# Performance work log

Hardware: AMD Instinct MI355X
Metric: run time of the kernel (lower is better)

Reference implementation:

```python
import jax, jax.numpy as jnp
import numpy as np

NB_FEAT = 20000
NB_CLASSES = 30
N_EDGES = 640000
BATCH = 128


def setup_inputs() -> dict:
    key = jax.random.key(0)
    k1, k2, k3, k4, k5 = jax.random.split(key, 5)
    x = jax.random.normal(k1, (BATCH, NB_FEAT), dtype=jnp.float32)
    edge_index = jax.random.randint(k2, (2, N_EDGES), 0, NB_FEAT, dtype=jnp.int64)
    edge_weight = jax.random.uniform(k3, (N_EDGES,), dtype=jnp.float32)
    fc_w = jax.random.normal(k4, (NB_CLASSES, NB_FEAT), dtype=jnp.float32) * 0.01
    fc_b = jax.random.normal(k5, (NB_CLASSES,), dtype=jnp.float32) * 0.01
    return {"x": x, "edge_index": edge_index, "edge_weight": edge_weight,
            "fc_w": fc_w, "fc_b": fc_b}


def reference(x, edge_index, edge_weight, fc_w, fc_b):
    # SGConv(K=1, bias=False, lin.weight frozen to 1) == gcn_norm + one propagation.
    B, N = x.shape
    src, dst = edge_index[0], edge_index[1]
    # add self-loops with weight 1 (gcn_norm default fill_value=1)
    loop = jnp.arange(N)
    src_f = jnp.concatenate([src, loop])
    dst_f = jnp.concatenate([dst, loop])
    w_f = jnp.concatenate([edge_weight, jnp.ones((N,), edge_weight.dtype)])
    # symmetric normalization: deg over target index
    deg = jax.ops.segment_sum(w_f, dst_f, num_segments=N)  # (N,)
    dinv = jnp.where(deg > 0, jax.lax.rsqrt(deg), 0.0)
    wn = dinv[src_f] * w_f * dinv[dst_f]  # (E',)
    # batched gather-multiply-scatter; graph shared across batch, so vectorize over B
    msgs = x[:, src_f] * wn  # (B, E')
    diffused = jax.ops.segment_sum(msgs.T, dst_f, num_segments=N).T  # (B, N)
    # dropout p=0 -> no-op; dense FC + softmax
    logits = diffused @ fc_w.T + fc_b  # (B, C)
    return jax.nn.softmax(logits, axis=1)
```

## Files before the change

kernel.cpp:

```cpp
#include <hip/hip_runtime.h>


#define N_NODES   20000
#define N_EDGES_C 640000
#define N_CLASSES 30
#define CPAD      32

#define HBLKS     32
#define HNODES    10000
#define HEDGES    (N_EDGES_C / HBLKS)

#define BN        32
#define NB        625
#define NSLAB     256
#define SLAB_E    (N_EDGES_C / NSLAB)
#define ECAP      1440

#define XLD       129
#define GTLD      33

__global__ __launch_bounds__(512) void k1_histscatter(const int* __restrict__ src,
        const int* __restrict__ dst, const float* __restrict__ ew,
        float* __restrict__ degp, int* __restrict__ gcur,
        int2* __restrict__ erec) {
    __shared__ union {
        float h[HNODES];
        struct { int ssrc[SLAB_E]; int shist[NB]; int scur[NB]; } s;
    } sm;
    int bid = blockIdx.x;
    int t = threadIdx.x;
    if (bid < 2 * HBLKS) {
        int eb = bid >> 1, half = bid & 1;
        int nbase = half * HNODES;
        for (int i = t; i < HNODES; i += 512) sm.h[i] = 0.f;
        __syncthreads();
        const int4* d4 = (const int4*)(dst + eb * HEDGES);
        const float4* w4 = (const float4*)(ew + eb * HEDGES);
        for (int i = t; i < HEDGES / 4; i += 512) {
            int4 dv = d4[i]; float4 wv = w4[i];
            unsigned r;
            r = (unsigned)(dv.x - nbase); if (r < HNODES) atomicAdd(&sm.h[r], wv.x);
            r = (unsigned)(dv.y - nbase); if (r < HNODES) atomicAdd(&sm.h[r], wv.y);
            r = (unsigned)(dv.z - nbase); if (r < HNODES) atomicAdd(&sm.h[r], wv.z);
            r = (unsigned)(dv.w - nbase); if (r < HNODES) atomicAdd(&sm.h[r], wv.w);
        }
        __syncthreads();
        float* outp = degp + (size_t)bid * HNODES;
        for (int i = t; i < HNODES; i += 512) outp[i] = sm.h[i];
    } else {
        int slab = bid - 2 * HBLKS;
        int e0 = slab * SLAB_E;
        for (int i = t; i < NB; i += 512) sm.s.shist[i] = 0;
        __syncthreads();
        const int4* s4 = (const int4*)(src + e0);
        for (int i = t; i < SLAB_E / 4; i += 512) {
            int4 sv = s4[i];
            ((int4*)sm.s.ssrc)[i] = sv;
            atomicAdd(&sm.s.shist[sv.x >> 5], 1);
            atomicAdd(&sm.s.shist[sv.y >> 5], 1);
            atomicAdd(&sm.s.shist[sv.z >> 5], 1);
            atomicAdd(&sm.s.shist[sv.w >> 5], 1);
        }
        __syncthreads();
        for (int b = t; b < NB; b += 512)
            sm.s.scur[b] = b * ECAP + atomicAdd(&gcur[b], sm.s.shist[b]);
        __syncthreads();
        const int4* d4 = (const int4*)(dst + e0);
        const float4* w4 = (const float4*)(ew + e0);
        for (int i = t; i < SLAB_E / 4; i += 512) {
            int4 dv = d4[i]; float4 wv = w4[i];
            int4 sv = ((const int4*)sm.s.ssrc)[i];
            int s, p;
            s = sv.x; p = atomicAdd(&sm.s.scur[s >> 5], 1);
            erec[p] = make_int2(((s & 31) << 15) | dv.x, __float_as_int(wv.x));
            s = sv.y; p = atomicAdd(&sm.s.scur[s >> 5], 1);
            erec[p] = make_int2(((s & 31) << 15) | dv.y, __float_as_int(wv.y));
            s = sv.z; p = atomicAdd(&sm.s.scur[s >> 5], 1);
            erec[p] = make_int2(((s & 31) << 15) | dv.z, __float_as_int(wv.z));
            s = sv.w; p = atomicAdd(&sm.s.scur[s >> 5], 1);
            erec[p] = make_int2(((s & 31) << 15) | dv.w, __float_as_int(wv.w));
        }
    }
}

__global__ __launch_bounds__(256) void k2_prep(const float* __restrict__ degp,
        const float* __restrict__ fc_w, float* __restrict__ dinv,
        float* __restrict__ fcT) {
    __shared__ float tile[CPAD][BN + 1];
    __shared__ float sdinv[BN];
    int n0 = blockIdx.x * BN;
    int t = threadIdx.x;
    if (t < BN) {
        int n = n0 + t;
        int half = n / HNODES, nn = n - half * HNODES;
        float s = 1.0f;
        for (int eb = 0; eb < HBLKS; eb++)
            s += degp[(size_t)((eb << 1) | half) * HNODES + nn];
        float di = rsqrtf(s);
        dinv[n] = di;
        sdinv[t] = di;
    }
    #pragma unroll
    for (int k = 0; k < 4; k++) {
        int idx = k * 256 + t;
        int c = idx >> 5, nn = idx & 31;
        tile[c][nn] = (c < N_CLASSES) ? fc_w[c * N_NODES + n0 + nn] : 0.f;
    }
    __syncthreads();
    #pragma unroll
    for (int k = 0; k < 4; k++) {
        int idx = k * 256 + t;
        int nn = idx >> 5, c = idx & 31;
        fcT[(size_t)(n0 + nn) * CPAD + c] = sdinv[nn] * tile[c][nn];
    }
}

__global__ __launch_bounds__(512) void k3_foldgemm(const int2* __restrict__ erec,
        const int* __restrict__ gcur, const float* __restrict__ dinv,
        const float* __restrict__ fcT, const float* __restrict__ x,
        float* __restrict__ part) {
    __shared__ union {
        struct { int2 srt[ECAP]; int hist[BN]; int rowst[BN]; int cur[BN]; } f;
        struct { float xl[BN * XLD]; float gt[CPAD * GTLD]; } g;
    } sm;
    float* gt = sm.g.gt;
    int bucket = blockIdx.x;
    int t = threadIdx.x;
    int nlo = bucket * BN;
    int bstart = bucket * ECAP;
    int len = min(gcur[bucket], ECAP);

    if (t < BN) sm.f.hist[t] = 0;
    __syncthreads();
    for (int i = t; i < len; i += 512)
        atomicAdd(&sm.f.hist[((unsigned)erec[bstart + i].x) >> 15], 1);
    __syncthreads();
    if (t < BN) {
        int h = sm.f.hist[t];
        int v = h;
        #pragma unroll
        for (int o = 1; o < BN; o <<= 1) {
            int u = __shfl_up(v, o, BN);
            if (t >= o) v += u;
        }
        sm.f.rowst[t] = v - h;
        sm.f.cur[t]   = v - h;
    }
    __syncthreads();
    for (int i = t; i < len; i += 512) {
        int2 r = erec[bstart + i];
        int p = atomicAdd(&sm.f.cur[((unsigned)r.x) >> 15], 1);
        sm.f.srt[p] = r;
    }
    __syncthreads();

    int c = t & 31;
    int grp = t >> 5;
    #pragma unroll
    for (int half = 0; half < 2; half++) {
        int nn = grp + half * 16;
        int n = nlo + nn;
        float acc  = fcT[(size_t)n * CPAD + c];
        float acc2 = 0.f;
        int i = sm.f.rowst[nn], re = i + sm.f.hist[nn];
        for (; i + 1 < re; i += 2) {
            int2 r0 = sm.f.srt[i], r1 = sm.f.srt[i + 1];
            acc  += __int_as_float(r0.y) * fcT[(size_t)(r0.x & 0x7FFF) * CPAD + c];
            acc2 += __int_as_float(r1.y) * fcT[(size_t)(r1.x & 0x7FFF) * CPAD + c];
        }
        if (i < re) {
            int2 r0 = sm.f.srt[i];
            acc += __int_as_float(r0.y) * fcT[(size_t)(r0.x & 0x7FFF) * CPAD + c];
        }
        gt[c * GTLD + nn] = dinv[n] * (acc + acc2);
    }
    __syncthreads();

    for (int o = t; o < 128 * BN; o += 512) {
        int b = o >> 5, n = o & 31;
        sm.g.xl[n * XLD + b] = x[(size_t)b * N_NODES + nlo + n];
    }
    __syncthreads();

    int wv = t >> 6, l = t & 63;
    float a00 = 0.f, a01 = 0.f, a10 = 0.f, a11 = 0.f;
    float a20 = 0.f, a21 = 0.f, a30 = 0.f, a31 = 0.f;
    #pragma unroll 8
    for (int n = 0; n < BN; n++) {
        float x0 = sm.g.xl[n * XLD + l];
        float x1 = sm.g.xl[n * XLD + 64 + l];
        float g0 = gt[(wv)      * GTLD + n];
        float g1 = gt[(wv +  8) * GTLD + n];
        float g2 = gt[(wv + 16) * GTLD + n];
        float g3 = gt[(wv + 24) * GTLD + n];
        a00 += x0 * g0; a01 += x1 * g0;
        a10 += x0 * g1; a11 += x1 * g1;
        a20 += x0 * g2; a21 += x1 * g2;
        a30 += x0 * g3; a31 += x1 * g3;
    }
    float* pb = part + (size_t)bucket * CPAD * 128;
    pb[(wv)      * 128 + l]      = a00;
    pb[(wv)      * 128 + 64 + l] = a01;
    pb[(wv +  8) * 128 + l]      = a10;
    pb[(wv +  8) * 128 + 64 + l] = a11;
    pb[(wv + 16) * 128 + l]      = a20;
    pb[(wv + 16) * 128 + 64 + l] = a21;
    pb[(wv + 24) * 128 + l]      = a30;
    pb[(wv + 24) * 128 + 64 + l] = a31;
}

__global__ __launch_bounds__(128) void k4_lred(const float* __restrict__ part,
        float* __restrict__ lpart) {
    int c = blockIdx.x, q = blockIdx.y;
    int b = threadIdx.x;
    float s = 0.f;
    for (int ch = q; ch < NB; ch += 5)
        s += part[(size_t)ch * CPAD * 128 + c * 128 + b];
    lpart[(q * CPAD + c) * 128 + b] = s;
}

__global__ void k5_smax(const float* __restrict__ lpart,
        const float* __restrict__ fc_b, float* __restrict__ out) {
    int b = threadIdx.x;
    float v[N_CLASSES], m = -1e30f;
    #pragma unroll
    for (int c = 0; c < N_CLASSES; c++) {
        float s = fc_b[c];
        #pragma unroll
        for (int q = 0; q < 5; q++) s += lpart[(q * CPAD + c) * 128 + b];
        v[c] = s; m = fmaxf(m, s);
    }
    float s = 0.f;
    #pragma unroll
    for (int c = 0; c < N_CLASSES; c++) { v[c] = __expf(v[c] - m); s += v[c]; }
    float inv = 1.0f / s;
    #pragma unroll
    for (int c = 0; c < N_CLASSES; c++) out[b * N_CLASSES + c] = v[c] * inv;
}

extern "C" void kernel_launch(void* const* d_in, const int* in_sizes, int n_in,
                              void* d_out, int out_size, void* d_ws, size_t ws_size,
                              hipStream_t stream) {
    const float* x          = (const float*)d_in[0];
    const int*   edge_index = (const int*)d_in[1];
    const float* ew         = (const float*)d_in[2];
    const float* fc_w       = (const float*)d_in[3];
    const float* fc_b       = (const float*)d_in[4];
    float* out = (float*)d_out;

    const int* src = edge_index;
    const int* dst = edge_index + N_EDGES_C;

    float* A     = (float*)d_ws;
    int2*  erec  = (int2*)(A + (size_t)NB * CPAD * 128);
    float* dinv  = (float*)(erec + (size_t)NB * ECAP);
    int*   gcur  = (int*)(dinv + N_NODES);
    float* fcT   = (float*)(gcur + 640);
    float* lpart = fcT + (size_t)N_NODES * CPAD;

    float* degp = A;
    float* part = A;

    hipMemsetAsync(gcur, 0, 640 * sizeof(int), stream);

    k1_histscatter<<<2 * HBLKS + NSLAB, 512, 0, stream>>>(src, dst, ew, degp,
                                                          gcur, erec);
    k2_prep<<<NB, 256, 0, stream>>>(degp, fc_w, dinv, fcT);
    k3_foldgemm<<<NB, 512, 0, stream>>>(erec, gcur, dinv, fcT, x, part);
    k4_lred<<<dim3(N_CLASSES, 5), 128, 0, stream>>>(part, lpart);
    k5_smax<<<1, 128, 0, stream>>>(lpart, fc_b, out);
}
```

Measured before the change: 96.14 us.

## Retune slab count, unroll gather by four, relayout partials, replace memset kernel

Raises the edge-slab block count in the histogram/scatter kernel, widens the k3 gather loop to four independent accumulators, and changes the partial-sum layout to class-major so each class's chunks are contiguous. The class reduction now runs over all chunks in one block per class and adds the bias there, leaving softmax to read finished logits. The memset is replaced by a tiny init kernel. Together these target launch overhead, latency hiding in the gather, and reduction access patterns. The trade-off is that the reduction uses only 30 blocks, giving less parallelism.

```diff
diff --git a/kernel.cpp b/kernel.cpp
--- a/kernel.cpp
+++ b/kernel.cpp
@@ -12,12 +12,17 @@
 
 #define BN        32
 #define NB        625
-#define NSLAB     256
+#define NSLAB     500
 #define SLAB_E    (N_EDGES_C / NSLAB)
 #define ECAP      1440
 
 #define XLD       129
 #define GTLD      33
+
+__global__ void k0_init(int* __restrict__ gcur) {
+    int t = threadIdx.x;
+    if (t < NB) gcur[t] = 0;
+}
 
 __global__ __launch_bounds__(512) void k1_histscatter(const int* __restrict__ src,
         const int* __restrict__ dst, const float* __restrict__ ew,
@@ -160,19 +165,22 @@
     for (int half = 0; half < 2; half++) {
         int nn = grp + half * 16;
         int n = nlo + nn;
-        float acc  = fcT[(size_t)n * CPAD + c];
-        float acc2 = 0.f;
+        float a0 = fcT[(size_t)n * CPAD + c];
+        float a1 = 0.f, a2 = 0.f, a3 = 0.f;
         int i = sm.f.rowst[nn], re = i + sm.f.hist[nn];
-        for (; i + 1 < re; i += 2) {
+        for (; i + 3 < re; i += 4) {
             int2 r0 = sm.f.srt[i], r1 = sm.f.srt[i + 1];
-            acc  += __int_as_float(r0.y) * fcT[(size_t)(r0.x & 0x7FFF) * CPAD + c];
-            acc2 += __int_as_float(r1.y) * fcT[(size_t)(r1.x & 0x7FFF) * CPAD + c];
-        }
-        if (i < re) {
+            int2 r2 = sm.f.srt[i + 2], r3 = sm.f.srt[i + 3];
+            a0 += __int_as_float(r0.y) * fcT[(size_t)(r0.x & 0x7FFF) * CPAD + c];
+            a1 += __int_as_float(r1.y) * fcT[(size_t)(r1.x & 0x7FFF) * CPAD + c];
+            a2 += __int_as_float(r2.y) * fcT[(size_t)(r2.x & 0x7FFF) * CPAD + c];
+            a3 += __int_as_float(r3.y) * fcT[(size_t)(r3.x & 0x7FFF) * CPAD + c];
+        }
+        for (; i < re; i++) {
             int2 r0 = sm.f.srt[i];
-            acc += __int_as_float(r0.y) * fcT[(size_t)(r0.x & 0x7FFF) * CPAD + c];
-        }
-        gt[c * GTLD + nn] = dinv[n] * (acc + acc2);
+            a0 += __int_as_float(r0.y) * fcT[(size_t)(r0.x & 0x7FFF) * CPAD + c];
+        }
+        gt[c * GTLD + nn] = dinv[n] * ((a0 + a1) + (a2 + a3));
     }
     __syncthreads();
 
@@ -198,37 +206,36 @@
         a20 += x0 * g2; a21 += x1 * g2;
         a30 += x0 * g3; a31 += x1 * g3;
     }
-    float* pb = part + (size_t)bucket * CPAD * 128;
-    pb[(wv)      * 128 + l]      = a00;
-    pb[(wv)      * 128 + 64 + l] = a01;
-    pb[(wv +  8) * 128 + l]      = a10;
-    pb[(wv +  8) * 128 + 64 + l] = a11;
-    pb[(wv + 16) * 128 + l]      = a20;
-    pb[(wv + 16) * 128 + 64 + l] = a21;
-    pb[(wv + 24) * 128 + l]      = a30;
-    pb[(wv + 24) * 128 + 64 + l] = a31;
+    part[((size_t)(wv)      * NB + bucket) * 128 + l]      = a00;
+    part[((size_t)(wv)      * NB + bucket) * 128 + 64 + l] = a01;
+    part[((size_t)(wv +  8) * NB + bucket) * 128 + l]      = a10;
+    part[((size_t)(wv +  8) * NB + bucket) * 128 + 64 + l] = a11;
+    part[((size_t)(wv + 16) * NB + bucket) * 128 + l]      = a20;
+    part[((size_t)(wv + 16) * NB + bucket) * 128 + 64 + l] = a21;
+    part[((size_t)(wv + 24) * NB + bucket) * 128 + l]      = a30;
+    part[((size_t)(wv + 24) * NB + bucket) * 128 + 64 + l] = a31;
 }
 
 __global__ __launch_bounds__(128) void k4_lred(const float* __restrict__ part,
-        float* __restrict__ lpart) {
-    int c = blockIdx.x, q = blockIdx.y;
+        const float* __restrict__ fc_b, float* __restrict__ logits_g) {
+    int c = blockIdx.x;
     int b = threadIdx.x;
+    const float* p = part + (size_t)c * NB * 128 + b;
     float s = 0.f;
-    for (int ch = q; ch < NB; ch += 5)
-        s += part[(size_t)ch * CPAD * 128 + c * 128 + b];
-    lpart[(q * CPAD + c) * 128 + b] = s;
-}
-
-__global__ void k5_smax(const float* __restrict__ lpart,
-        const float* __restrict__ fc_b, float* __restrict__ out) {
+    #pragma unroll 8
+    for (int ch = 0; ch < NB; ch++)
+        s += p[(size_t)ch * 128];
+    logits_g[b * CPAD + c] = s + fc_b[c];
+}
+
+__global__ void k5_smax(const float* __restrict__ logits_g,
+        float* __restrict__ out) {
     int b = threadIdx.x;
     float v[N_CLASSES], m = -1e30f;
     #pragma unroll
     for (int c = 0; c < N_CLASSES; c++) {
-        float s = fc_b[c];
-        #pragma unroll
-        for (int q = 0; q < 5; q++) s += lpart[(q * CPAD + c) * 128 + b];
-        v[c] = s; m = fmaxf(m, s);
+        v[c] = logits_g[b * CPAD + c];
+        m = fmaxf(m, v[c]);
     }
     float s = 0.f;
     #pragma unroll
@@ -251,22 +258,21 @@
     const int* src = edge_index;
     const int* dst = edge_index + N_EDGES_C;
 
-    float* A     = (float*)d_ws;
-    int2*  erec  = (int2*)(A + (size_t)NB * CPAD * 128);
-    float* dinv  = (float*)(erec + (size_t)NB * ECAP);
-    int*   gcur  = (int*)(dinv + N_NODES);
-    float* fcT   = (float*)(gcur + 640);
-    float* lpart = fcT + (size_t)N_NODES * CPAD;
+    float* A        = (float*)d_ws;
+    int2*  erec     = (int2*)(A + (size_t)NB * CPAD * 128);
+    float* dinv     = (float*)(erec + (size_t)NB * ECAP);
+    int*   gcur     = (int*)(dinv + N_NODES);
+    float* fcT      = (float*)(gcur + 640);
+    float* logits_g = fcT + (size_t)N_NODES * CPAD;
 
     float* degp = A;
     float* part = A;
 
-    hipMemsetAsync(gcur, 0, 640 * sizeof(int), stream);
-
+    k0_init<<<1, 640, 0, stream>>>(gcur);
     k1_histscatter<<<2 * HBLKS + NSLAB, 512, 0, stream>>>(src, dst, ew, degp,
                                                           gcur, erec);
     k2_prep<<<NB, 256, 0, stream>>>(degp, fc_w, dinv, fcT);
     k3_foldgemm<<<NB, 512, 0, stream>>>(erec, gcur, dinv, fcT, x, part);
-    k4_lred<<<dim3(N_CLASSES, 5), 128, 0, stream>>>(part, lpart);
-    k5_smax<<<1, 128, 0, stream>>>(lpart, fc_b, out);
-}
+    k4_lred<<<N_CLASSES, 128, 0, stream>>>(part, fc_b, logits_g);
+    k5_smax<<<1, 128, 0, stream>>>(logits_g, out);
+}
```

Measured after the change: 107.8 us. 1.12x slower.
